# Kernel optimization log

Measured on AMD Instinct MI355X. Metric: run time of the kernel, lower is better.

Reference implementation:

```python
import jax, jax.numpy as jnp
import numpy as np

N, H, D, HDIM, HID = 768, 4, 3, 64, 64


def setup_inputs() -> dict:
    key = jax.random.key(0)
    ks = jax.random.split(key, 12)

    def w(k, shape, scale=None):
        s = (1.0 / np.sqrt(shape[0])) if scale is None else scale
        return (jax.random.normal(k, shape, jnp.float32) * s).astype(jnp.float32)

    d_in_e = H + 2 * (HDIM + H * H)  # 4 + 2*(64+16) = 164
    return {
        "x": jax.random.normal(ks[0], (N, H, D), jnp.float32),
        "h": jax.random.normal(ks[1], (N, HDIM), jnp.float32),
        "phi_e_w0": w(ks[2], (d_in_e, HID)), "phi_e_b0": jnp.zeros((HID,), jnp.float32),
        "phi_e_w1": w(ks[3], (HID, HID)), "phi_e_b1": jnp.zeros((HID,), jnp.float32),
        "phi_inf_w": w(ks[4], (HID, 1)), "phi_inf_b": jnp.zeros((1,), jnp.float32),
        "phi_x_w0": w(ks[5], (HID, HID)), "phi_x_b0": jnp.zeros((HID,), jnp.float32),
        "phi_x_w1": w(ks[6], (HID, HID)), "phi_x_b1": jnp.zeros((HID,), jnp.float32),
        "phi_x_w2": w(ks[7], (HID, H), scale=0.001), "phi_x_b2": jnp.zeros((H,), jnp.float32),
        "phi_h_w0": w(ks[8], (HID + HDIM, HID)), "phi_h_b0": jnp.zeros((HID,), jnp.float32),
        "phi_h_w1": w(ks[9], (HID, HID)), "phi_h_b1": jnp.zeros((HID,), jnp.float32),
        "phi_h_w2": w(ks[10], (HID, HDIM)), "phi_h_b2": jnp.zeros((HDIM,), jnp.float32),
    }


def _mlp2(z, w0, b0, w1, b1):
    # hk.nets.MLP([HID, HID], activation=silu, activate_final=True)
    return jax.nn.silu(jax.nn.silu(z @ w0 + b0) @ w1 + b1)


def reference(x, h,
              phi_e_w0, phi_e_b0, phi_e_w1, phi_e_b1,
              phi_inf_w, phi_inf_b,
              phi_x_w0, phi_x_b0, phi_x_w1, phi_x_b1, phi_x_w2, phi_x_b2,
              phi_h_w0, phi_h_b0, phi_h_w1, phi_h_b1, phi_h_w2, phi_h_b2):
    n, n_heads = x.shape[0], x.shape[1]
    avg_num_neighbours = n - 1
    off_n = 1.0 - jnp.eye(n, dtype=x.dtype)          # zero node-diagonal mask

    # per-node head-pair differences: [n, H, H, 3], entry [m,i,j] = x[m,j]-x[m,i]
    diff_heads = x[:, None, :, :] - x[:, :, None, :]
    sq_norms_heads = jnp.sum(diff_heads ** 2, axis=-1)            # [n, H, H]
    h_concat = jnp.concatenate([h, sq_norms_heads.reshape(n, n_heads * n_heads)], axis=-1)

    # all-pairs node features: [n, n, 2*(HDIM+H^2)], entry [i,j] = [h_concat[j], h_concat[i]]
    hc_dim = h_concat.shape[-1]
    h_combos = jnp.concatenate([
        jnp.broadcast_to(h_concat[None, :, :], (n, n, hc_dim)),
        jnp.broadcast_to(h_concat[:, None, :], (n, n, hc_dim)),
    ], axis=-1)

    # all-pairs node differences per head: [n, n, H, 3], entry [i,j] = x[j]-x[i]
    diff_nodes = x[None, :, :, :] - x[:, None, :, :]
    sq_norms_nodes = jnp.sum(diff_nodes ** 2, axis=-1)            # [n, n, H]

    e_in = jnp.concatenate([sq_norms_nodes, h_combos], axis=-1)   # [n, n, 164]
    m_ij = _mlp2(e_in, phi_e_w0, phi_e_b0, phi_e_w1, phi_e_b1)    # [n, n, HID]
    m_ij = m_ij * off_n[:, :, None]

    e = jax.nn.sigmoid(m_ij @ phi_inf_w + phi_inf_b)[..., 0] * off_n  # [n, n]
    m_i = jnp.einsum('ijd,ij->id', m_ij, e) / jnp.sqrt(jnp.asarray(avg_num_neighbours, x.dtype))

    # phi_x: MLP(silu, activate_final) -> Linear(H) (tanh=False)
    phi_x_out = (_mlp2(m_ij, phi_x_w0, phi_x_b0, phi_x_w1, phi_x_b1) @ phi_x_w2 + phi_x_b2)
    phi_x_out = phi_x_out * off_n[:, :, None]                     # [n, n, H]

    # normalize_by_x_norm=True, normalization_constant=1.0
    norm = jnp.sqrt(jnp.where(sq_norms_nodes == 0.0, 1.0, sq_norms_nodes)) + 1.0
    norm_diff = (diff_nodes / norm[..., None]) * off_n[:, :, None, None]
    equivariant_shift = jnp.einsum('ijhd,ijh->ihd', norm_diff, phi_x_out)
    equivariant_shift = equivariant_shift / avg_num_neighbours    # agg='mean'

    x_new = x + equivariant_shift

    phi_h_in = jnp.concatenate([m_i, h], axis=-1)
    h_new = _mlp2(phi_h_in, phi_h_w0, phi_h_b0, phi_h_w1, phi_h_b1) @ phi_h_w2 + phi_h_b2
    h_new = h + h_new                                             # residual_h=True
    return (x_new, h_new)
```

## Files before the change

### kernel.cpp

```cpp
#include <hip/hip_runtime.h>
#include <hip/hip_bf16.h>
#include <math.h>

#define WS_BJ    0
#define WS_BI    49152
#define WS_W0AT  98304
#define WS_BIAS  98560
#define WS_INFW  98784
#define WS_WG    98848
#define WS_PM    106016
#define WS_PS    155168

typedef unsigned short ushort_t;
typedef __attribute__((ext_vector_type(8))) __bf16 bf16x8;
typedef __attribute__((ext_vector_type(4))) float f32x4;

__device__ __forceinline__ float silu_f(float v) {
    return v * __builtin_amdgcn_rcpf(1.0f + __expf(-v));
}
__device__ __forceinline__ float sigm_f(float v) {
    return __builtin_amdgcn_rcpf(1.0f + __expf(-v));
}

__device__ __forceinline__ ushort_t bf16r(float f) {
    unsigned u = __float_as_uint(f);
    u += 0x7FFFu + ((u >> 16) & 1u);
    return (ushort_t)(u >> 16);
}

__device__ __forceinline__ unsigned pk2(float a, float b) {
    __hip_bfloat162 t = __float22bfloat162_rn(make_float2(a, b));
    return *reinterpret_cast<unsigned*>(&t);
}

__global__ __launch_bounds__(256) void prep_kernel(
    const float* __restrict__ x, const float* __restrict__ h,
    const float* __restrict__ ew0, const float* __restrict__ eb0,
    const float* __restrict__ ew1, const float* __restrict__ eb1,
    const float* __restrict__ infw, const float* __restrict__ infb,
    const float* __restrict__ xw0, const float* __restrict__ xb0,
    const float* __restrict__ xw1, const float* __restrict__ xb1,
    const float* __restrict__ xw2, const float* __restrict__ xb2,
    float* __restrict__ ws)
{
    const int blk = blockIdx.x, tid = threadIdx.x;
    const int wv = tid >> 6, t = tid & 63;
    if (blk < 192) {
        __shared__ float hcs[4][80];
        const int m = blk * 4 + wv;
        hcs[wv][t] = h[m * 64 + t];
        if (t < 16) {
            int i2 = t >> 2, j2 = t & 3;
            float d0 = x[m*12 + j2*3 + 0] - x[m*12 + i2*3 + 0];
            float d1 = x[m*12 + j2*3 + 1] - x[m*12 + i2*3 + 1];
            float d2 = x[m*12 + j2*3 + 2] - x[m*12 + i2*3 + 2];
            hcs[wv][64 + t] = d0*d0 + d1*d1 + d2*d2;
        }
        float bj = 0.0f, bi = eb0[t];
        #pragma unroll 4
        for (int k = 0; k < 80; ++k) {
            float hv = hcs[wv][k];
            bj += hv * ew0[(4 + k) * 64 + t];
            bi += hv * ew0[(84 + k) * 64 + t];
        }
        ws[WS_BJ + m * 64 + t] = bj;
        ws[WS_BI + m * 64 + t] = bi;
    } else if (blk == 192) {
        if (wv == 0) {
            #pragma unroll
            for (int hh = 0; hh < 4; ++hh) ws[WS_W0AT + t * 4 + hh] = ew0[hh * 64 + t];
            ws[WS_INFW + t] = infw[t];
            #pragma unroll
            for (int u = 0; u < 4; ++u) {
                int idx = u * 64 + t;
                if (idx < 224) {
                    float v;
                    if (idx < 64)        v = eb1[idx];
                    else if (idx < 128)  v = xb0[idx - 64];
                    else if (idx == 128) v = infb[0];
                    else if (idx < 144)  v = 0.0f;
                    else if (idx < 208)  v = xb1[idx - 144];
                    else if (idx < 212)  v = xb2[idx - 208];
                    else                 v = 0.0f;
                    ws[WS_BIAS + idx] = v;
                }
            }
        }
    } else if (blk < 200) {
        ushort_t* wg = (ushort_t*)(ws + WS_WG);
        #pragma unroll 1
        for (int u = 0; u < 8; ++u) {
            int e = (blk - 193) * 2048 + tid * 8 + u;
            int r = e >> 6, k = e & 63;
            float v;
            if (r < 64)        v = ew1[k * 64 + r];
            else if (r < 128)  v = xw0[k * 64 + (r - 64)];
            else if (r == 128) v = infw[k];
            else if (r < 144)  v = 0.0f;
            else if (r < 208)  v = xw1[k * 64 + (r - 144)];
            else if (r < 212)  v = xw2[k * 4 + (r - 208)];
            else               v = 0.0f;
            wg[e] = bf16r(v);
        }
    } else {
        int e = (blk - 200) * 256 + tid;
        if (e < 58368) ws[WS_PM + e] = 0.0f;
    }
}

__device__ __forceinline__ void load_bfrags(const ushort_t* yb, int ml, int q, bf16x8 B[4][2]) {
    #pragma unroll
    for (int pt = 0; pt < 4; ++pt)
        #pragma unroll
        for (int kt = 0; kt < 2; ++kt)
            B[pt][kt] = *(const bf16x8*)(yb + (pt*16 + ml) * 72 + kt*32 + q*8);
}

template<int NMT>
__device__ __forceinline__ void gemmG(const ushort_t* __restrict__ wg, int ml, int q,
                                      const bf16x8 B[4][2], f32x4* acc) {
    #pragma unroll
    for (int mt = 0; mt < NMT; ++mt) {
        #pragma unroll
        for (int kt = 0; kt < 2; ++kt) {
            bf16x8 af = *(const bf16x8*)(wg + (mt*16 + ml) * 64 + kt*32 + q*8);
            #pragma unroll
            for (int pt = 0; pt < 4; ++pt)
                acc[mt*4 + pt] = __builtin_amdgcn_mfma_f32_16x16x32_bf16(af, B[pt][kt], acc[mt*4 + pt], 0, 0, 0);
        }
    }
}

__device__ __forceinline__ void acc_bias(f32x4* acc, const float* __restrict__ bias,
                                         int coff, int q) {
    #pragma unroll
    for (int mt = 0; mt < 2; ++mt) {
        float4 bv = *(const float4*)(bias + coff + mt*16 + q*4);
        #pragma unroll
        for (int pt = 0; pt < 4; ++pt)
            acc[mt*4 + pt] = f32x4{bv.x, bv.y, bv.z, bv.w};
    }
}

__device__ __forceinline__ void layer64B(ushort_t* yb, const ushort_t* __restrict__ wg,
                                         const float* __restrict__ bias, int ml, int q,
                                         const bf16x8 B[4][2]) {
    f32x4 acc[8];
    #pragma unroll
    for (int half = 0; half < 2; ++half) {
        acc_bias(acc, bias, half*32, q);
        gemmG<2>(wg + half*32*64, ml, q, B, acc);
        #pragma unroll
        for (int mt = 0; mt < 2; ++mt) {
            #pragma unroll
            for (int pt = 0; pt < 4; ++pt) {
                f32x4 a = acc[mt*4 + pt];
                uint2 w = make_uint2(pk2(silu_f(a[0]), silu_f(a[1])),
                                     pk2(silu_f(a[2]), silu_f(a[3])));
                *(uint2*)(yb + (pt*16 + ml) * 72 + half*32 + mt*16 + q*4) = w;
            }
        }
    }
}

__global__ __launch_bounds__(256, 2) void egcl_chunk(
    const float* __restrict__ x, float* __restrict__ ws)
{
    __shared__ ushort_t ybuf[4][4608];

    const int it = blockIdx.x, i = blockIdx.y, tid = threadIdx.x;
    const int wv = tid >> 6, lane = tid & 63;
    const int ml = lane & 15, q = lane >> 4;
    const int jg = it * 256 + wv * 64 + lane;

    const ushort_t* wg = (const ushort_t*)(ws + WS_WG);
    const float* bias  = ws + WS_BIAS;
    const float* infwf = ws + WS_INFW;
    ushort_t* yb = ybuf[wv];

    float xi[12];
    #pragma unroll
    for (int t = 0; t < 12; ++t) xi[t] = x[i * 12 + t];

    float sqn[4];
    {
        const float4* xp = (const float4*)(x + jg * 12);
        float4 a = xp[0], b = xp[1], c = xp[2];
        float d0, d1, d2;
        d0=a.x-xi[0]; d1=a.y-xi[1]; d2=a.z-xi[2];   sqn[0]=d0*d0+d1*d1+d2*d2;
        d0=a.w-xi[3]; d1=b.x-xi[4]; d2=b.y-xi[5];   sqn[1]=d0*d0+d1*d1+d2*d2;
        d0=b.z-xi[6]; d1=b.w-xi[7]; d2=c.x-xi[8];   sqn[2]=d0*d0+d1*d1+d2*d2;
        d0=c.y-xi[9]; d1=c.z-xi[10];d2=c.w-xi[11];  sqn[3]=d0*d0+d1*d1+d2*d2;
    }

    {
        const float* Bi   = ws + WS_BI + i * 64;
        const float* w0at = ws + WS_W0AT;
        const float* Bj   = ws + WS_BJ + jg * 64;
        #pragma unroll
        for (int b = 0; b < 8; ++b) {
            float4 A = *(const float4*)(Bj + b*8);
            float4 Bv = *(const float4*)(Bj + b*8 + 4);
            float z[8] = {A.x, A.y, A.z, A.w, Bv.x, Bv.y, Bv.z, Bv.w};
            #pragma unroll
            for (int u = 0; u < 8; ++u) {
                int l = b*8 + u;
                float v = Bi[l] + z[u]
                        + sqn[0]*w0at[l*4+0] + sqn[1]*w0at[l*4+1]
                        + sqn[2]*w0at[l*4+2] + sqn[3]*w0at[l*4+3];
                z[u] = silu_f(v);
            }
            uint4 pkv = make_uint4(pk2(z[0],z[1]), pk2(z[2],z[3]),
                                   pk2(z[4],z[5]), pk2(z[6],z[7]));
            *(uint4*)(yb + lane * 72 + b*8) = pkv;
        }
    }

    bf16x8 B[4][2];

    float infp[4] = {0.f, 0.f, 0.f, 0.f};
    {
        load_bfrags(yb, ml, q, B);
        f32x4 acc[8];
        #pragma unroll
        for (int half = 0; half < 2; ++half) {
            acc_bias(acc, bias + 0, half*32, q);
            gemmG<2>(wg + half*32*64, ml, q, B, acc);
            #pragma unroll
            for (int mt = 0; mt < 2; ++mt) {
                float4 iw = *(const float4*)(infwf + half*32 + mt*16 + q*4);
                #pragma unroll
                for (int pt = 0; pt < 4; ++pt) {
                    f32x4 a = acc[mt*4 + pt];
                    float s0 = silu_f(a[0]), s1 = silu_f(a[1]);
                    float s2 = silu_f(a[2]), s3 = silu_f(a[3]);
                    infp[pt] += s0*iw.x + s1*iw.y + s2*iw.z + s3*iw.w;
                    *(uint2*)(yb + (pt*16 + ml) * 72 + half*32 + mt*16 + q*4) =
                        make_uint2(pk2(s0, s1), pk2(s2, s3));
                }
            }
        }
    }

    float e4[4];
    {
        float binf = bias[128];
        #pragma unroll
        for (int pt = 0; pt < 4; ++pt) {
            float v = infp[pt];
            v += __shfl_xor(v, 16, 64);
            v += __shfl_xor(v, 32, 64);
            int jp = it * 256 + wv * 64 + pt*16 + ml;
            e4[pt] = (jp == i) ? 0.0f : sigm_f(v + binf);
        }
    }

    float macc[16];
    load_bfrags(yb, ml, q, B);
    #pragma unroll
    for (int kt = 0; kt < 2; ++kt) {
        #pragma unroll
        for (int j = 0; j < 8; ++j) {
            float s = e4[0] * (float)B[0][kt][j];
            s      += e4[1] * (float)B[1][kt][j];
            s      += e4[2] * (float)B[2][kt][j];
            s      += e4[3] * (float)B[3][kt][j];
            macc[kt*8 + j] = s;
        }
    }
    layer64B(yb, wg + 64*64, bias + 64, ml, q, B);

    load_bfrags(yb, ml, q, B);
    layer64B(yb, wg + 144*64, bias + 144, ml, q, B);

    float* yf = (float*)yb;
    {
        load_bfrags(yb, ml, q, B);
        f32x4 acc2[4];
        {
            float4 bx2 = *(const float4*)(bias + 208);
            #pragma unroll
            for (int pt = 0; pt < 4; ++pt) acc2[pt] = f32x4{bx2.x, bx2.y, bx2.z, bx2.w};
        }
        gemmG<1>(wg + 208*64, ml, q, B, acc2);
        if (q == 0) {
            #pragma unroll
            for (int pt = 0; pt < 4; ++pt)
                *(float4*)(yf + (pt*16 + ml) * 4) =
                    make_float4(acc2[pt][0], acc2[pt][1], acc2[pt][2], acc2[pt][3]);
        }
    }

    {
        float4 pv = *(const float4*)(yf + lane * 4);
        float pvh[4] = {pv.x, pv.y, pv.z, pv.w};
        float mask = (jg == i) ? 0.0f : 1.0f;
        const float4* xp = (const float4*)(x + jg * 12);
        float4 a = xp[0], b = xp[1], c = xp[2];
        float dxs[12];
        dxs[0]=a.x-xi[0]; dxs[1]=a.y-xi[1]; dxs[2]=a.z-xi[2];  dxs[3]=a.w-xi[3];
        dxs[4]=b.x-xi[4]; dxs[5]=b.y-xi[5]; dxs[6]=b.z-xi[6];  dxs[7]=b.w-xi[7];
        dxs[8]=c.x-xi[8]; dxs[9]=c.y-xi[9]; dxs[10]=c.z-xi[10];dxs[11]=c.w-xi[11];
        float s12[12];
        #pragma unroll
        for (int hh = 0; hh < 4; ++hh) {
            float nsq = (sqn[hh] == 0.0f) ? 1.0f : sqn[hh];
            float inv = mask * pvh[hh] * __builtin_amdgcn_rcpf(sqrtf(nsq) + 1.0f);
            #pragma unroll
            for (int d = 0; d < 3; ++d)
                s12[hh*3 + d] = dxs[hh*3 + d] * inv;
        }
        #pragma unroll
        for (int t = 0; t < 12; ++t) {
            float v = s12[t];
            v += __shfl_xor(v, 1, 64);
            v += __shfl_xor(v, 2, 64);
            v += __shfl_xor(v, 4, 64);
            v += __shfl_xor(v, 8, 64);
            v += __shfl_xor(v, 16, 64);
            v += __shfl_xor(v, 32, 64);
            if (lane == 0) atomicAdd(&ws[WS_PS + i*12 + t], v);
        }
    }

    #pragma unroll
    for (int s = 0; s < 16; ++s) {
        float v = macc[s];
        v += __shfl_xor(v, 1, 64);
        v += __shfl_xor(v, 2, 64);
        v += __shfl_xor(v, 4, 64);
        v += __shfl_xor(v, 8, 64);
        macc[s] = v;
    }
    if (ml == 0) {
        #pragma unroll
        for (int kt = 0; kt < 2; ++kt)
            #pragma unroll
            for (int j = 0; j < 8; ++j)
                atomicAdd(&ws[WS_PM + i*64 + kt*32 + q*8 + j], macc[kt*8 + j]);
    }
}

__global__ __launch_bounds__(64) void finish_kernel(
    const float* __restrict__ x, const float* __restrict__ h,
    const float* __restrict__ hw0, const float* __restrict__ hb0,
    const float* __restrict__ hw1, const float* __restrict__ hb1,
    const float* __restrict__ hw2, const float* __restrict__ hb2,
    const float* __restrict__ ws, float* __restrict__ out)
{
    __shared__ float inbuf[128];
    __shared__ float zbuf[64];
    const int i = blockIdx.x, lane = threadIdx.x;

    float mi = ws[WS_PM + i*64 + lane] * (1.0f / sqrtf(767.0f));
    inbuf[lane] = mi;
    inbuf[64 + lane] = h[i*64 + lane];

    if (lane < 12) {
        float sh = ws[WS_PS + i*12 + lane];
        out[i*12 + lane] = x[i*12 + lane] + sh * (1.0f / 767.0f);
    }

    float a = hb0[lane];
    #pragma unroll 8
    for (int k = 0; k < 128; ++k) a += inbuf[k] * hw0[k*64 + lane];
    zbuf[lane] = silu_f(a);

    a = hb1[lane];
    #pragma unroll 8
    for (int k = 0; k < 64; ++k) a += zbuf[k] * hw1[k*64 + lane];
    zbuf[lane] = silu_f(a);

    a = hb2[lane];
    #pragma unroll 8
    for (int k = 0; k < 64; ++k) a += zbuf[k] * hw2[k*64 + lane];
    out[9216 + i*64 + lane] = h[i*64 + lane] + a;
}

extern "C" void kernel_launch(void* const* d_in, const int* in_sizes, int n_in,
                              void* d_out, int out_size, void* d_ws, size_t ws_size,
                              hipStream_t stream) {
    const float* x    = (const float*)d_in[0];
    const float* h    = (const float*)d_in[1];
    const float* ew0  = (const float*)d_in[2];
    const float* eb0  = (const float*)d_in[3];
    const float* ew1  = (const float*)d_in[4];
    const float* eb1  = (const float*)d_in[5];
    const float* infw = (const float*)d_in[6];
    const float* infb = (const float*)d_in[7];
    const float* xw0  = (const float*)d_in[8];
    const float* xb0  = (const float*)d_in[9];
    const float* xw1  = (const float*)d_in[10];
    const float* xb1  = (const float*)d_in[11];
    const float* xw2  = (const float*)d_in[12];
    const float* xb2  = (const float*)d_in[13];
    const float* hw0  = (const float*)d_in[14];
    const float* hb0  = (const float*)d_in[15];
    const float* hw1  = (const float*)d_in[16];
    const float* hb1  = (const float*)d_in[17];
    const float* hw2  = (const float*)d_in[18];
    const float* hb2  = (const float*)d_in[19];

    float* ws  = (float*)d_ws;
    float* out = (float*)d_out;

    prep_kernel<<<428, 256, 0, stream>>>(x, h, ew0, eb0, ew1, eb1, infw, infb,
                                         xw0, xb0, xw1, xb1, xw2, xb2, ws);
    egcl_chunk<<<dim3(3, 768), 256, 0, stream>>>(x, ws);
    finish_kernel<<<768, 64, 0, stream>>>(x, h, hw0, hb0, hw1, hb1, hw2, hb2, ws, out);
}
```

Measured before the change: 190.9 us.

## Replace global atomics with per-block partial sums reduced in finish kernel

Each egcl_chunk block now reduces its m_i and shift contributions across waves in shared memory and writes one partial per (node, chunk), instead of issuing many global atomicAdds per wave. finish_kernel sums the three chunk partials, so the zeroing blocks in prep_kernel are dropped. The m_i accumulation is also rewritten as a per-lane loop over shared-memory attention weights instead of holding a B fragment across layers, which lowers register pressure at the cost of more LDS reads and a block barrier.

Measured after the change: 176.9 us. 7.3% less time.

```diff
diff --git a/kernel.cpp b/kernel.cpp
--- a/kernel.cpp
+++ b/kernel.cpp
@@ -9,7 +9,7 @@
 #define WS_INFW  98784
 #define WS_WG    98848
 #define WS_PM    106016
-#define WS_PS    155168
+#define WS_PS    253472
 
 typedef unsigned short ushort_t;
 typedef __attribute__((ext_vector_type(8))) __bf16 bf16x8;
@@ -27,6 +27,7 @@
     u += 0x7FFFu + ((u >> 16) & 1u);
     return (ushort_t)(u >> 16);
 }
+__device__ __forceinline__ float bf2f(ushort_t s) { return __uint_as_float(((unsigned)s) << 16); }
 
 __device__ __forceinline__ unsigned pk2(float a, float b) {
     __hip_bfloat162 t = __float22bfloat162_rn(make_float2(a, b));
@@ -86,7 +87,7 @@
                 }
             }
         }
-    } else if (blk < 200) {
+    } else {
         ushort_t* wg = (ushort_t*)(ws + WS_WG);
         #pragma unroll 1
         for (int u = 0; u < 8; ++u) {
@@ -102,9 +103,6 @@
             else               v = 0.0f;
             wg[e] = bf16r(v);
         }
-    } else {
-        int e = (blk - 200) * 256 + tid;
-        if (e < 58368) ws[WS_PM + e] = 0.0f;
     }
 }
 
@@ -142,9 +140,10 @@
     }
 }
 
-__device__ __forceinline__ void layer64B(ushort_t* yb, const ushort_t* __restrict__ wg,
-                                         const float* __restrict__ bias, int ml, int q,
-                                         const bf16x8 B[4][2]) {
+__device__ __forceinline__ void layer64(ushort_t* yb, const ushort_t* __restrict__ wg,
+                                        const float* __restrict__ bias, int ml, int q) {
+    bf16x8 B[4][2];
+    load_bfrags(yb, ml, q, B);
     f32x4 acc[8];
     #pragma unroll
     for (int half = 0; half < 2; ++half) {
@@ -167,6 +166,9 @@
     const float* __restrict__ x, float* __restrict__ ws)
 {
     __shared__ ushort_t ybuf[4][4608];
+    __shared__ float sbuf[4][64];
+    __shared__ float redm[4][64];
+    __shared__ float reds[4][12];
 
     const int it = blockIdx.x, i = blockIdx.y, tid = threadIdx.x;
     const int wv = tid >> 6, lane = tid & 63;
@@ -216,11 +218,10 @@
         }
     }
 
-    bf16x8 B[4][2];
-
-    float infp[4] = {0.f, 0.f, 0.f, 0.f};
-    {
+    {
+        bf16x8 B[4][2];
         load_bfrags(yb, ml, q, B);
+        float infp[4] = {0.f, 0.f, 0.f, 0.f};
         f32x4 acc[8];
         #pragma unroll
         for (int half = 0; half < 2; ++half) {
@@ -240,10 +241,6 @@
                 }
             }
         }
-    }
-
-    float e4[4];
-    {
         float binf = bias[128];
         #pragma unroll
         for (int pt = 0; pt < 4; ++pt) {
@@ -251,30 +248,24 @@
             v += __shfl_xor(v, 16, 64);
             v += __shfl_xor(v, 32, 64);
             int jp = it * 256 + wv * 64 + pt*16 + ml;
-            e4[pt] = (jp == i) ? 0.0f : sigm_f(v + binf);
-        }
-    }
-
-    float macc[16];
-    load_bfrags(yb, ml, q, B);
-    #pragma unroll
-    for (int kt = 0; kt < 2; ++kt) {
-        #pragma unroll
-        for (int j = 0; j < 8; ++j) {
-            float s = e4[0] * (float)B[0][kt][j];
-            s      += e4[1] * (float)B[1][kt][j];
-            s      += e4[2] * (float)B[2][kt][j];
-            s      += e4[3] * (float)B[3][kt][j];
-            macc[kt*8 + j] = s;
-        }
-    }
-    layer64B(yb, wg + 64*64, bias + 64, ml, q, B);
-
-    load_bfrags(yb, ml, q, B);
-    layer64B(yb, wg + 144*64, bias + 144, ml, q, B);
+            float ea = (jp == i) ? 0.0f : sigm_f(v + binf);
+            if (q == 0) sbuf[wv][pt*16 + ml] = ea;
+        }
+    }
+
+    float macc = 0.0f;
+    #pragma unroll 8
+    for (int j2 = 0; j2 < 64; ++j2) {
+        float ev = sbuf[wv][j2];
+        macc += ev * bf2f(yb[j2 * 72 + lane]);
+    }
+
+    layer64(yb, wg + 64*64, bias + 64, ml, q);
+    layer64(yb, wg + 144*64, bias + 144, ml, q);
 
     float* yf = (float*)yb;
     {
+        bf16x8 B[4][2];
         load_bfrags(yb, ml, q, B);
         f32x4 acc2[4];
         {
@@ -319,25 +310,19 @@
             v += __shfl_xor(v, 8, 64);
             v += __shfl_xor(v, 16, 64);
             v += __shfl_xor(v, 32, 64);
-            if (lane == 0) atomicAdd(&ws[WS_PS + i*12 + t], v);
-        }
-    }
-
-    #pragma unroll
-    for (int s = 0; s < 16; ++s) {
-        float v = macc[s];
-        v += __shfl_xor(v, 1, 64);
-        v += __shfl_xor(v, 2, 64);
-        v += __shfl_xor(v, 4, 64);
-        v += __shfl_xor(v, 8, 64);
-        macc[s] = v;
-    }
-    if (ml == 0) {
-        #pragma unroll
-        for (int kt = 0; kt < 2; ++kt)
-            #pragma unroll
-            for (int j = 0; j < 8; ++j)
-                atomicAdd(&ws[WS_PM + i*64 + kt*32 + q*8 + j], macc[kt*8 + j]);
+            if (lane == 0) reds[wv][t] = v;
+        }
+    }
+
+    redm[wv][lane] = macc;
+    __syncthreads();
+
+    if (wv == 0) {
+        ws[WS_PM + (i*3 + it)*64 + lane] =
+            redm[0][lane] + redm[1][lane] + redm[2][lane] + redm[3][lane];
+        if (lane < 12)
+            ws[WS_PS + (i*3 + it)*12 + lane] =
+                reds[0][lane] + reds[1][lane] + reds[2][lane] + reds[3][lane];
     }
 }
 
@@ -352,12 +337,14 @@
     __shared__ float zbuf[64];
     const int i = blockIdx.x, lane = threadIdx.x;
 
-    float mi = ws[WS_PM + i*64 + lane] * (1.0f / sqrtf(767.0f));
+    const float* pm = ws + WS_PM + i*3*64;
+    float mi = (pm[lane] + pm[64 + lane] + pm[128 + lane]) * (1.0f / sqrtf(767.0f));
     inbuf[lane] = mi;
     inbuf[64 + lane] = h[i*64 + lane];
 
     if (lane < 12) {
-        float sh = ws[WS_PS + i*12 + lane];
+        const float* ps = ws + WS_PS + i*3*12;
+        float sh = ps[lane] + ps[12 + lane] + ps[24 + lane];
         out[i*12 + lane] = x[i*12 + lane] + sh * (1.0f / 767.0f);
     }
 
@@ -404,7 +391,7 @@
     float* ws  = (float*)d_ws;
     float* out = (float*)d_out;
 
-    prep_kernel<<<428, 256, 0, stream>>>(x, h, ew0, eb0, ew1, eb1, infw, infb,
+    prep_kernel<<<200, 256, 0, stream>>>(x, h, ew0, eb0, ew1, eb1, infw, infb,
                                          xw0, xb0, xw1, xb1, xw2, xb2, ws);
     egcl_chunk<<<dim3(3, 768), 256, 0, stream>>>(x, ws);
     finish_kernel<<<768, 64, 0, stream>>>(x, h, hw0, hb0, hw1, hb1, hw2, hb2, ws, out);
```
